# Performance work log

Measured on AMD Instinct MI355X. Metric: run time of the kernel, lower is better.

The kernel has to match this reference:

```python
import jax, jax.numpy as jnp
import numpy as np


def setup_inputs() -> dict:
    key = jax.random.key(0)
    k1, k2, k3 = jax.random.split(key, 3)
    B, C, H, W = 16, 512, 64, 64
    K = 32
    std = 1.0 / (K * C) ** 0.5
    x = jax.random.normal(k1, (B, C, H, W), dtype=jnp.float32)
    codewords = jax.random.uniform(k2, (K, C), dtype=jnp.float32, minval=-std, maxval=std)
    scale = jax.random.uniform(k3, (K,), dtype=jnp.float32, minval=-1.0, maxval=0.0)
    return {"x": x, "codewords": codewords, "scale": scale}


def reference(x, codewords, scale):
    # x: [B, C, H, W] -> tokens [B, N, C] with N = H*W
    B, C, H, W = x.shape
    xf = x.reshape(B, C, H * W).transpose(0, 2, 1)  # [B, N, C]

    # (avoids materializing the [B, N, K, C] tensor the torch code builds)
    x_sq = jnp.sum(xf * xf, axis=-1)                 # [B, N]
    c_sq = jnp.sum(codewords * codewords, axis=-1)   # [K]
    xc = jnp.einsum('bnc,kc->bnk', xf, codewords)    # [B, N, K]
    scaled_l2 = scale * (x_sq[..., None] - 2.0 * xc + c_sq)  # [B, N, K]

    w = jax.nn.softmax(scaled_l2, axis=2)            # [B, N, K]

    # aggregate: sum_n w[b,n,k] * (x[b,n,:] - c[k,:])
    #          = einsum(w, x) - (sum_n w) * c
    enc = jnp.einsum('bnk,bnc->bkc', w, xf) - jnp.sum(w, axis=1)[..., None] * codewords
    return enc  # [B, K, C]
```

## Files before the change

### kernel.cpp

```cpp
#include <hip/hip_runtime.h>


#define B_ 16
#define C_ 512
#define N_ 4096
#define K_ 32
#define CWS 520
#define WLS 40
#define XCP 132

typedef __attribute__((ext_vector_type(8))) short short8;
typedef __attribute__((ext_vector_type(16))) float floatx16;

__device__ inline unsigned short f2bf(float f) {
    union { float f; unsigned u; } v; v.f = f;
    unsigned r = v.u + 0x7FFFu + ((v.u >> 16) & 1u);
    return (unsigned short)(r >> 16);
}
__device__ inline float bf2f(unsigned short s) {
    union { unsigned u; float f; } v; v.u = ((unsigned)s) << 16;
    return v.f;
}

template <int USE_WS>
__global__ __launch_bounds__(256, 2)
void enc_kernel(const float* __restrict__ x, const float* __restrict__ cw,
                const float* __restrict__ scale, float* __restrict__ outp)
{
    __shared__ unsigned short cwT[K_ * CWS];
    __shared__ unsigned short XC[2][64 * XCP];
    __shared__ unsigned short Wl[4][K_ * WLS];
    __shared__ float xsqp[4][128];
    __shared__ float csq[K_];
    __shared__ float scl[K_];

    const int tid  = threadIdx.x;
    const int wave = tid >> 6;
    const int lane = tid & 63;
    const int l31  = lane & 31;
    const int lh   = lane >> 5;

    const int b     = blockIdx.x >> 5;
    const int chunk = blockIdx.x & 31;
    const float* xb = x + (long)b * C_ * N_;

    const int r = tid >> 5;
    const int p = tid & 31;
    const float* xrow = xb + chunk * 128 + p * 4;

    float4 sA[8], sB[8];
#define XISSUE(buf_, g_)                                                       \
    { _Pragma("unroll")                                                        \
      for (int i = 0; i < 8; ++i)                                              \
          buf_[i] = *(const float4*)(xrow + (long)((g_) * 64 + i * 8 + r) * N_); }

    float xs0 = 0.f, xs1 = 0.f, xs2 = 0.f, xs3 = 0.f;
#define XWRITE(buf_, dst_)                                                     \
    { _Pragma("unroll")                                                        \
      for (int i = 0; i < 8; ++i) {                                            \
          const float4 v = buf_[i];                                            \
          xs0 += v.x * v.x; xs1 += v.y * v.y;                                  \
          xs2 += v.z * v.z; xs3 += v.w * v.w;                                  \
          const unsigned lo = (unsigned)f2bf(v.x) | ((unsigned)f2bf(v.y) << 16);\
          const unsigned hi = (unsigned)f2bf(v.z) | ((unsigned)f2bf(v.w) << 16);\
          *(uint2*)&XC[dst_][(i * 8 + r) * XCP + p * 4] = make_uint2(lo, hi);  \
      } }

    XISSUE(sA, 0)
    XISSUE(sB, 1)

    if (tid < K_) scl[tid] = scale[tid];
    {
        const int k = tid >> 3, q = tid & 7;
        const float4* src = (const float4*)(cw + k * C_ + q * 64);
        float s = 0.f;
        #pragma unroll
        for (int i = 0; i < 16; ++i) {
            const float4 v = src[i];
            s += v.x*v.x + v.y*v.y + v.z*v.z + v.w*v.w;
            const unsigned lo = (unsigned)f2bf(v.x) | ((unsigned)f2bf(v.y) << 16);
            const unsigned hi = (unsigned)f2bf(v.z) | ((unsigned)f2bf(v.w) << 16);
            *(uint2*)&cwT[k * CWS + q * 64 + i * 4] = make_uint2(lo, hi);
        }
        s += __shfl_xor(s, 1); s += __shfl_xor(s, 2); s += __shfl_xor(s, 4);
        if (q == 0) csq[k] = s;
    }

    XWRITE(sA, 0)
    __syncthreads();

    floatx16 S;
    #pragma unroll
    for (int i = 0; i < 16; ++i) S[i] = 0.f;

    #pragma unroll
    for (int g = 0; g < 8; ++g) {
        if (g + 2 < 8) {
            if ((g & 1) == 0) { XISSUE(sA, g + 2) } else { XISSUE(sB, g + 2) }
        }
        #pragma unroll
        for (int s = 0; s < 4; ++s) {
            const short8 af = *(const short8*)&cwT[l31 * CWS + (g * 4 + s) * 16 + lh * 8];
            short8 bx;
            #pragma unroll
            for (int j = 0; j < 8; ++j)
                bx[j] = (short)XC[g & 1][(s * 16 + lh * 8 + j) * XCP + wave * 32 + l31];
            S = __builtin_amdgcn_mfma_f32_32x32x16_bf16(af, bx, S, 0, 0, 0);
        }
        if (g + 1 < 8) {
            if ((g & 1) == 0) { XWRITE(sB, (g + 1) & 1) } else { XWRITE(sA, (g + 1) & 1) }
        }
        if (g < 7) __syncthreads();
    }

    xs0 += __shfl_xor(xs0, 32); xs1 += __shfl_xor(xs1, 32);
    xs2 += __shfl_xor(xs2, 32); xs3 += __shfl_xor(xs3, 32);
    if (lane < 32) {
        xsqp[wave][l31 * 4 + 0] = xs0; xsqp[wave][l31 * 4 + 1] = xs1;
        xsqp[wave][l31 * 4 + 2] = xs2; xsqp[wave][l31 * 4 + 3] = xs3;
    }

    float4 bv[6][2];
#define G2LOAD(bi_, i_)                                                        \
    { const int t_ = (i_) >> 3, st_ = (i_) & 7;                                \
      const int c_ = wave * 128 + t_ * 32 + l31;                               \
      const int no_ = (st_ >> 1) * 32 + (st_ & 1) * 16 + lh * 8;               \
      const float* p_ = xb + (long)c_ * N_ + chunk * 128 + no_;                \
      bv[bi_][0] = *(const float4*)p_;                                         \
      bv[bi_][1] = *(const float4*)(p_ + 4); }
    G2LOAD(0, 0)
    G2LOAD(1, 1)
    G2LOAD(2, 2)
    G2LOAD(3, 3)
    G2LOAD(4, 4)
    G2LOAD(5, 5)

    __syncthreads();

    {
        const int n = wave * 32 + l31;
        const float xq = xsqp[0][n] + xsqp[1][n] + xsqp[2][n] + xsqp[3][n];
        float L[16], mx = -3.4e38f;
        #pragma unroll
        for (int rr = 0; rr < 16; ++rr) {
            const int k = (rr & 3) + 8 * (rr >> 2) + 4 * lh;
            L[rr] = scl[k] * (xq - 2.f * S[rr] + csq[k]);
            mx = fmaxf(mx, L[rr]);
        }
        mx = fmaxf(mx, __shfl_xor(mx, 32));
        float sum = 0.f;
        #pragma unroll
        for (int rr = 0; rr < 16; ++rr) { L[rr] = __expf(L[rr] - mx); sum += L[rr]; }
        sum += __shfl_xor(sum, 32);
        const float inv = 1.f / sum;
        #pragma unroll
        for (int rr = 0; rr < 16; ++rr) {
            const int k = (rr & 3) + 8 * (rr >> 2) + 4 * lh;
            Wl[wave][k * WLS + l31] = f2bf(L[rr] * inv);
        }
    }
    __syncthreads();

    short8 aw[8];
    #pragma unroll
    for (int st = 0; st < 8; ++st)
        aw[st] = *(const short8*)&Wl[st >> 1][l31 * WLS + (st & 1) * 16 + lh * 8];

    floatx16 wacc;
    #pragma unroll
    for (int i = 0; i < 16; ++i) wacc[i] = 0.f;
    {
        short8 ones;
        #pragma unroll
        for (int j = 0; j < 8; ++j) ones[j] = (short)0x3F80;
        #pragma unroll
        for (int st = 0; st < 8; ++st)
            wacc = __builtin_amdgcn_mfma_f32_32x32x16_bf16(aw[st], ones, wacc, 0, 0, 0);
    }

    floatx16 acc[4];
    #pragma unroll
    for (int t = 0; t < 4; ++t)
        #pragma unroll
        for (int i = 0; i < 16; ++i) acc[t][i] = 0.f;

    #pragma unroll
    for (int i = 0; i < 32; ++i) {
        const int bi = i % 6;
        const int t  = i >> 3, st = i & 7;
        const float4 v0 = bv[bi][0];
        const float4 v1 = bv[bi][1];
        short8 bx;
        bx[0] = (short)f2bf(v0.x); bx[1] = (short)f2bf(v0.y);
        bx[2] = (short)f2bf(v0.z); bx[3] = (short)f2bf(v0.w);
        bx[4] = (short)f2bf(v1.x); bx[5] = (short)f2bf(v1.y);
        bx[6] = (short)f2bf(v1.z); bx[7] = (short)f2bf(v1.w);
        acc[t] = __builtin_amdgcn_mfma_f32_32x32x16_bf16(aw[st], bx, acc[t], 0, 0, 0);
        if (i + 6 < 32) G2LOAD(bi, i + 6)
    }

    float* dst = USE_WS ? (outp + (size_t)blockIdx.x * K_ * C_)
                        : (outp + (size_t)b * K_ * C_);
    #pragma unroll
    for (int t = 0; t < 4; ++t) {
        const int c = wave * 128 + t * 32 + l31;
        #pragma unroll
        for (int rr = 0; rr < 16; ++rr) {
            const int k = (rr & 3) + 8 * (rr >> 2) + 4 * lh;
            const float cwv = bf2f(cwT[k * CWS + c]);
            const float val = acc[t][rr] - wacc[rr] * cwv;
            if (USE_WS) dst[k * C_ + c] = val;
            else        atomicAdd(dst + k * C_ + c, val);
        }
    }
}

__global__ __launch_bounds__(256)
void reduce_kernel(const float4* __restrict__ part, float4* __restrict__ out)
{
    const int gid = blockIdx.x * 256 + threadIdx.x;
    const int bb  = gid >> 12;
    const int i4  = gid & 4095;
    const float4* p = part + ((size_t)bb * 32) * 4096 + i4;
    float4 s = make_float4(0.f, 0.f, 0.f, 0.f);
    #pragma unroll
    for (int ch = 0; ch < 32; ++ch) {
        const float4 v = p[(size_t)ch * 4096];
        s.x += v.x; s.y += v.y; s.z += v.z; s.w += v.w;
    }
    out[gid] = s;
}

extern "C" void kernel_launch(void* const* d_in, const int* in_sizes, int n_in,
                              void* d_out, int out_size, void* d_ws, size_t ws_size,
                              hipStream_t stream) {
    const float* x     = (const float*)d_in[0];
    const float* cw    = (const float*)d_in[1];
    const float* scale = (const float*)d_in[2];
    float* out = (float*)d_out;

    const size_t ws_need = (size_t)512 * K_ * C_ * sizeof(float);
    if (ws_size >= ws_need) {
        float* part = (float*)d_ws;
        hipLaunchKernelGGL(enc_kernel<1>, dim3(B_ * 32), dim3(256), 0, stream,
                           x, cw, scale, part);
        hipLaunchKernelGGL(reduce_kernel, dim3(256), dim3(256), 0, stream,
                           (const float4*)part, (float4*)out);
    } else {
        hipMemsetAsync(out, 0, (size_t)out_size * sizeof(float), stream);
        hipLaunchKernelGGL(enc_kernel<0>, dim3(B_ * 32), dim3(256), 0, stream,
                           x, cw, scale, out);
    }
}
```

Baseline: 216.7 us.

## Halve token chunk, keep whole x tile in LDS, precompute bf16 codewords

Token chunk per block drops from 128 to 64, doubling the block count to 1024. The full 512x64 bf16 x tile now stays resident in LDS, so the aggregation GEMM reads it from LDS instead of re-reading x from global memory a second time. Codeword bf16 conversion and norms move to a tiny separate kernel, and the distance MFMAs run on two waves that load A fragments from global. The trade-offs are an extra launch, a partial-sum workspace twice as large for the reduce kernel, and idle waves during the first GEMM.

```diff
diff --git a/kernel.cpp b/kernel.cpp
--- a/kernel.cpp
+++ b/kernel.cpp
@@ -5,9 +5,11 @@
 #define C_ 512
 #define N_ 4096
 #define K_ 32
-#define CWS 520
+#define CHUNK 64
+#define NCH (N_ / CHUNK)
+#define NBLK (B_ * NCH)
+#define XCP 72
 #define WLS 40
-#define XCP 132
 
 typedef __attribute__((ext_vector_type(8))) short short8;
 typedef __attribute__((ext_vector_type(16))) float floatx16;
@@ -17,20 +19,39 @@
     unsigned r = v.u + 0x7FFFu + ((v.u >> 16) & 1u);
     return (unsigned short)(r >> 16);
 }
-__device__ inline float bf2f(unsigned short s) {
-    union { unsigned u; float f; } v; v.u = ((unsigned)s) << 16;
-    return v.f;
+
+__global__ __launch_bounds__(256)
+void cw_convert(const float* __restrict__ cw, unsigned short* __restrict__ cwb,
+                float* __restrict__ csq)
+{
+    const int tid = threadIdx.x;
+    const int k = tid >> 3, q = tid & 7;
+    const float4* src = (const float4*)(cw + k * C_ + q * 64);
+    float s = 0.f;
+    #pragma unroll
+    for (int i = 0; i < 16; ++i) {
+        const float4 v = src[i];
+        s += v.x*v.x + v.y*v.y + v.z*v.z + v.w*v.w;
+        const unsigned lo = (unsigned)f2bf(v.x) | ((unsigned)f2bf(v.y) << 16);
+        const unsigned hi = (unsigned)f2bf(v.z) | ((unsigned)f2bf(v.w) << 16);
+        *(uint2*)&cwb[k * C_ + q * 64 + i * 4] = make_uint2(lo, hi);
+    }
+    s += __shfl_xor(s, 1); s += __shfl_xor(s, 2); s += __shfl_xor(s, 4);
+    if (q == 0) csq[k] = s;
 }
 
 template <int USE_WS>
 __global__ __launch_bounds__(256, 2)
-void enc_kernel(const float* __restrict__ x, const float* __restrict__ cw,
-                const float* __restrict__ scale, float* __restrict__ outp)
+void enc_kernel(const float* __restrict__ x,
+                const unsigned short* __restrict__ cwb,
+                const float* __restrict__ csqg,
+                const float* __restrict__ cw,
+                const float* __restrict__ scale,
+                float* __restrict__ outp)
 {
-    __shared__ unsigned short cwT[K_ * CWS];
-    __shared__ unsigned short XC[2][64 * XCP];
-    __shared__ unsigned short Wl[4][K_ * WLS];
-    __shared__ float xsqp[4][128];
+    __shared__ unsigned short XC[C_ * XCP];
+    __shared__ unsigned short Wl[2][K_ * WLS];
+    __shared__ float xsqp[4][CHUNK];
     __shared__ float csq[K_];
     __shared__ float scl[K_];
 
@@ -40,53 +61,46 @@
     const int l31  = lane & 31;
     const int lh   = lane >> 5;
 
-    const int b     = blockIdx.x >> 5;
-    const int chunk = blockIdx.x & 31;
+    const int b     = blockIdx.x >> 6;
+    const int chunk = blockIdx.x & (NCH - 1);
     const float* xb = x + (long)b * C_ * N_;
 
-    const int r = tid >> 5;
-    const int p = tid & 31;
-    const float* xrow = xb + chunk * 128 + p * 4;
-
-    float4 sA[8], sB[8];
+    const int r = tid >> 4;
+    const int p = tid & 15;
+    const float* xrow = xb + chunk * CHUNK + p * 4;
+
+    if (tid < K_) { scl[tid] = scale[tid]; csq[tid] = csqg[tid]; }
+
+    float4 s0[4], s1[4], s2[4];
 #define XISSUE(buf_, g_)                                                       \
     { _Pragma("unroll")                                                        \
-      for (int i = 0; i < 8; ++i)                                              \
-          buf_[i] = *(const float4*)(xrow + (long)((g_) * 64 + i * 8 + r) * N_); }
+      for (int i = 0; i < 4; ++i)                                              \
+          buf_[i] = *(const float4*)(xrow + (long)((g_) * 64 + i * 16 + r) * N_); }
 
     float xs0 = 0.f, xs1 = 0.f, xs2 = 0.f, xs3 = 0.f;
-#define XWRITE(buf_, dst_)                                                     \
+#define XWRITE(buf_, g_)                                                       \
     { _Pragma("unroll")                                                        \
-      for (int i = 0; i < 8; ++i) {                                            \
+      for (int i = 0; i < 4; ++i) {                                            \
           const float4 v = buf_[i];                                            \
           xs0 += v.x * v.x; xs1 += v.y * v.y;                                  \
           xs2 += v.z * v.z; xs3 += v.w * v.w;                                  \
           const unsigned lo = (unsigned)f2bf(v.x) | ((unsigned)f2bf(v.y) << 16);\
           const unsigned hi = (unsigned)f2bf(v.z) | ((unsigned)f2bf(v.w) << 16);\
-          *(uint2*)&XC[dst_][(i * 8 + r) * XCP + p * 4] = make_uint2(lo, hi);  \
+          *(uint2*)&XC[((g_) * 64 + i * 16 + r) * XCP + p * 4] = make_uint2(lo, hi);\
       } }
 
-    XISSUE(sA, 0)
-    XISSUE(sB, 1)
-
-    if (tid < K_) scl[tid] = scale[tid];
-    {
-        const int k = tid >> 3, q = tid & 7;
-        const float4* src = (const float4*)(cw + k * C_ + q * 64);
-        float s = 0.f;
-        #pragma unroll
-        for (int i = 0; i < 16; ++i) {
-            const float4 v = src[i];
-            s += v.x*v.x + v.y*v.y + v.z*v.z + v.w*v.w;
-            const unsigned lo = (unsigned)f2bf(v.x) | ((unsigned)f2bf(v.y) << 16);
-            const unsigned hi = (unsigned)f2bf(v.z) | ((unsigned)f2bf(v.w) << 16);
-            *(uint2*)&cwT[k * CWS + q * 64 + i * 4] = make_uint2(lo, hi);
-        }
-        s += __shfl_xor(s, 1); s += __shfl_xor(s, 2); s += __shfl_xor(s, 4);
-        if (q == 0) csq[k] = s;
-    }
-
-    XWRITE(sA, 0)
+    const unsigned short* cwr = cwb + l31 * C_ + lh * 8;
+    short8 afA[4], afB[4];
+#define AFLOAD(buf_, g_)                                                       \
+    { _Pragma("unroll")                                                        \
+      for (int s = 0; s < 4; ++s)                                              \
+          buf_[s] = *(const short8*)(cwr + (g_) * 64 + s * 16); }
+
+    XISSUE(s0, 0)
+    XISSUE(s1, 1)
+    if (wave < 2) AFLOAD(afA, 0)
+    XWRITE(s0, 0)
+    XISSUE(s2, 2)
     __syncthreads();
 
     floatx16 S;
@@ -95,49 +109,44 @@
 
     #pragma unroll
     for (int g = 0; g < 8; ++g) {
-        if (g + 2 < 8) {
-            if ((g & 1) == 0) { XISSUE(sA, g + 2) } else { XISSUE(sB, g + 2) }
-        }
-        #pragma unroll
-        for (int s = 0; s < 4; ++s) {
-            const short8 af = *(const short8*)&cwT[l31 * CWS + (g * 4 + s) * 16 + lh * 8];
-            short8 bx;
+        if (g + 3 < 8) {
+            if      ((g % 3) == 0) XISSUE(s0, g + 3)
+            else if ((g % 3) == 1) XISSUE(s1, g + 3)
+            else                   XISSUE(s2, g + 3)
+        }
+        if (wave < 2) {
+            if (g + 1 < 8) {
+                if (g & 1) AFLOAD(afA, g + 1) else AFLOAD(afB, g + 1)
+            }
             #pragma unroll
-            for (int j = 0; j < 8; ++j)
-                bx[j] = (short)XC[g & 1][(s * 16 + lh * 8 + j) * XCP + wave * 32 + l31];
-            S = __builtin_amdgcn_mfma_f32_32x32x16_bf16(af, bx, S, 0, 0, 0);
+            for (int s = 0; s < 4; ++s) {
+                short8 bx;
+                #pragma unroll
+                for (int j = 0; j < 8; ++j)
+                    bx[j] = (short)XC[(g * 64 + s * 16 + lh * 8 + j) * XCP + wave * 32 + l31];
+                S = __builtin_amdgcn_mfma_f32_32x32x16_bf16((g & 1) ? afB[s] : afA[s],
+                                                            bx, S, 0, 0, 0);
+            }
         }
         if (g + 1 < 8) {
-            if ((g & 1) == 0) { XWRITE(sB, (g + 1) & 1) } else { XWRITE(sA, (g + 1) & 1) }
+            if      (((g + 1) % 3) == 0) XWRITE(s0, g + 1)
+            else if (((g + 1) % 3) == 1) XWRITE(s1, g + 1)
+            else                         XWRITE(s2, g + 1)
         }
         if (g < 7) __syncthreads();
     }
 
+    xs0 += __shfl_xor(xs0, 16); xs1 += __shfl_xor(xs1, 16);
+    xs2 += __shfl_xor(xs2, 16); xs3 += __shfl_xor(xs3, 16);
     xs0 += __shfl_xor(xs0, 32); xs1 += __shfl_xor(xs1, 32);
     xs2 += __shfl_xor(xs2, 32); xs3 += __shfl_xor(xs3, 32);
-    if (lane < 32) {
-        xsqp[wave][l31 * 4 + 0] = xs0; xsqp[wave][l31 * 4 + 1] = xs1;
-        xsqp[wave][l31 * 4 + 2] = xs2; xsqp[wave][l31 * 4 + 3] = xs3;
-    }
-
-    float4 bv[6][2];
-#define G2LOAD(bi_, i_)                                                        \
-    { const int t_ = (i_) >> 3, st_ = (i_) & 7;                                \
-      const int c_ = wave * 128 + t_ * 32 + l31;                               \
-      const int no_ = (st_ >> 1) * 32 + (st_ & 1) * 16 + lh * 8;               \
-      const float* p_ = xb + (long)c_ * N_ + chunk * 128 + no_;                \
-      bv[bi_][0] = *(const float4*)p_;                                         \
-      bv[bi_][1] = *(const float4*)(p_ + 4); }
-    G2LOAD(0, 0)
-    G2LOAD(1, 1)
-    G2LOAD(2, 2)
-    G2LOAD(3, 3)
-    G2LOAD(4, 4)
-    G2LOAD(5, 5)
-
+    if (lane < 16) {
+        xsqp[wave][lane * 4 + 0] = xs0; xsqp[wave][lane * 4 + 1] = xs1;
+        xsqp[wave][lane * 4 + 2] = xs2; xsqp[wave][lane * 4 + 3] = xs3;
+    }
     __syncthreads();
 
-    {
+    if (wave < 2) {
         const int n = wave * 32 + l31;
         const float xq = xsqp[0][n] + xsqp[1][n] + xsqp[2][n] + xsqp[3][n];
         float L[16], mx = -3.4e38f;
@@ -161,10 +170,10 @@
     }
     __syncthreads();
 
-    short8 aw[8];
-    #pragma unroll
-    for (int st = 0; st < 8; ++st)
-        aw[st] = *(const short8*)&Wl[st >> 1][l31 * WLS + (st & 1) * 16 + lh * 8];
+    short8 aw[4];
+    #pragma unroll
+    for (int s = 0; s < 4; ++s)
+        aw[s] = *(const short8*)&Wl[s >> 1][l31 * WLS + (s & 1) * 16 + lh * 8];
 
     floatx16 wacc;
     #pragma unroll
@@ -174,8 +183,8 @@
         #pragma unroll
         for (int j = 0; j < 8; ++j) ones[j] = (short)0x3F80;
         #pragma unroll
-        for (int st = 0; st < 8; ++st)
-            wacc = __builtin_amdgcn_mfma_f32_32x32x16_bf16(aw[st], ones, wacc, 0, 0, 0);
+        for (int s = 0; s < 4; ++s)
+            wacc = __builtin_amdgcn_mfma_f32_32x32x16_bf16(aw[s], ones, wacc, 0, 0, 0);
     }
 
     floatx16 acc[4];
@@ -185,18 +194,13 @@
         for (int i = 0; i < 16; ++i) acc[t][i] = 0.f;
 
     #pragma unroll
-    for (int i = 0; i < 32; ++i) {
-        const int bi = i % 6;
-        const int t  = i >> 3, st = i & 7;
-        const float4 v0 = bv[bi][0];
-        const float4 v1 = bv[bi][1];
-        short8 bx;
-        bx[0] = (short)f2bf(v0.x); bx[1] = (short)f2bf(v0.y);
-        bx[2] = (short)f2bf(v0.z); bx[3] = (short)f2bf(v0.w);
-        bx[4] = (short)f2bf(v1.x); bx[5] = (short)f2bf(v1.y);
-        bx[6] = (short)f2bf(v1.z); bx[7] = (short)f2bf(v1.w);
-        acc[t] = __builtin_amdgcn_mfma_f32_32x32x16_bf16(aw[st], bx, acc[t], 0, 0, 0);
-        if (i + 6 < 32) G2LOAD(bi, i + 6)
+    for (int t = 0; t < 4; ++t) {
+        const int c = wave * 128 + t * 32 + l31;
+        #pragma unroll
+        for (int s = 0; s < 4; ++s) {
+            const short8 bx = *(const short8*)&XC[c * XCP + s * 16 + lh * 8];
+            acc[t] = __builtin_amdgcn_mfma_f32_32x32x16_bf16(aw[s], bx, acc[t], 0, 0, 0);
+        }
     }
 
     float* dst = USE_WS ? (outp + (size_t)blockIdx.x * K_ * C_)
@@ -207,8 +211,7 @@
         #pragma unroll
         for (int rr = 0; rr < 16; ++rr) {
             const int k = (rr & 3) + 8 * (rr >> 2) + 4 * lh;
-            const float cwv = bf2f(cwT[k * CWS + c]);
-            const float val = acc[t][rr] - wacc[rr] * cwv;
+            const float val = acc[t][rr] - wacc[rr] * cw[k * C_ + c];
             if (USE_WS) dst[k * C_ + c] = val;
             else        atomicAdd(dst + k * C_ + c, val);
         }
@@ -221,10 +224,10 @@
     const int gid = blockIdx.x * 256 + threadIdx.x;
     const int bb  = gid >> 12;
     const int i4  = gid & 4095;
-    const float4* p = part + ((size_t)bb * 32) * 4096 + i4;
+    const float4* p = part + ((size_t)bb * NCH) * 4096 + i4;
     float4 s = make_float4(0.f, 0.f, 0.f, 0.f);
-    #pragma unroll
-    for (int ch = 0; ch < 32; ++ch) {
+    #pragma unroll 8
+    for (int ch = 0; ch < NCH; ++ch) {
         const float4 v = p[(size_t)ch * 4096];
         s.x += v.x; s.y += v.y; s.z += v.z; s.w += v.w;
     }
@@ -239,16 +242,22 @@
     const float* scale = (const float*)d_in[2];
     float* out = (float*)d_out;
 
-    const size_t ws_need = (size_t)512 * K_ * C_ * sizeof(float);
+    unsigned short* cwb = (unsigned short*)d_ws;
+    float* csq = (float*)((char*)d_ws + (size_t)K_ * C_ * sizeof(unsigned short));
+    const size_t part_off = 65536;
+    const size_t ws_need = part_off + (size_t)NBLK * K_ * C_ * sizeof(float);
+
     if (ws_size >= ws_need) {
-        float* part = (float*)d_ws;
-        hipLaunchKernelGGL(enc_kernel<1>, dim3(B_ * 32), dim3(256), 0, stream,
-                           x, cw, scale, part);
+        float* part = (float*)((char*)d_ws + part_off);
+        hipLaunchKernelGGL(cw_convert, dim3(1), dim3(256), 0, stream, cw, cwb, csq);
+        hipLaunchKernelGGL(enc_kernel<1>, dim3(NBLK), dim3(256), 0, stream,
+                           x, cwb, csq, cw, scale, part);
         hipLaunchKernelGGL(reduce_kernel, dim3(256), dim3(256), 0, stream,
                            (const float4*)part, (float4*)out);
     } else {
         hipMemsetAsync(out, 0, (size_t)out_size * sizeof(float), stream);
-        hipLaunchKernelGGL(enc_kernel<0>, dim3(B_ * 32), dim3(256), 0, stream,
-                           x, cw, scale, out);
-    }
-}
+        hipLaunchKernelGGL(cw_convert, dim3(1), dim3(256), 0, stream, cw, cwb, csq);
+        hipLaunchKernelGGL(enc_kernel<0>, dim3(NBLK), dim3(256), 0, stream,
+                           x, cwb, csq, cw, scale, out);
+    }
+}
```

Result: slower. 222.9 us (+2.9%).

## Drop LDS staging; load x and codewords directly from global into MFMA operands

Applied to the files above, without the earlier changes.

Removes the shared-memory staging of bf16 x tiles and the transposed codeword table. Each lane now loads its x column elements and codeword fragments straight from global memory, converting to bf16 in registers, and computes the x-squared norm per lane, which eliminates the cross-wave xsqp reduction. This frees LDS so occupancy can rise to 3 blocks per CU, and replaces __syncthreads with lighter custom barriers. The cost is strided scalar global loads for x (one float per row, 8 rows per MFMA) with no software prefetch, and redundant codeword reads across waves, which may expose memory latency.

```diff
diff --git a/kernel.cpp b/kernel.cpp
--- a/kernel.cpp
+++ b/kernel.cpp
@@ -5,9 +5,10 @@
 #define C_ 512
 #define N_ 4096
 #define K_ 32
-#define CWS 520
+#define CHUNK 128
+#define NCH (N_ / CHUNK)
+#define NBLK (B_ * NCH)
 #define WLS 40
-#define XCP 132
 
 typedef __attribute__((ext_vector_type(8))) short short8;
 typedef __attribute__((ext_vector_type(16))) float floatx16;
@@ -17,20 +18,22 @@
     unsigned r = v.u + 0x7FFFu + ((v.u >> 16) & 1u);
     return (unsigned short)(r >> 16);
 }
-__device__ inline float bf2f(unsigned short s) {
-    union { unsigned u; float f; } v; v.u = ((unsigned)s) << 16;
-    return v.f;
+
+__device__ inline void cbar() {
+    __builtin_amdgcn_sched_barrier(0);
+    asm volatile("s_waitcnt lgkmcnt(0)" ::: "memory");
+    __builtin_amdgcn_s_barrier();
+    __builtin_amdgcn_sched_barrier(0);
 }
 
 template <int USE_WS>
-__global__ __launch_bounds__(256, 2)
-void enc_kernel(const float* __restrict__ x, const float* __restrict__ cw,
-                const float* __restrict__ scale, float* __restrict__ outp)
+__global__ __launch_bounds__(256, 3)
+void enc_kernel(const float* __restrict__ x,
+                const float* __restrict__ cw,
+                const float* __restrict__ scale,
+                float* __restrict__ outp)
 {
-    __shared__ unsigned short cwT[K_ * CWS];
-    __shared__ unsigned short XC[2][64 * XCP];
     __shared__ unsigned short Wl[4][K_ * WLS];
-    __shared__ float xsqp[4][128];
     __shared__ float csq[K_];
     __shared__ float scl[K_];
 
@@ -41,91 +44,79 @@
     const int lh   = lane >> 5;
 
     const int b     = blockIdx.x >> 5;
-    const int chunk = blockIdx.x & 31;
+    const int chunk = blockIdx.x & (NCH - 1);
     const float* xb = x + (long)b * C_ * N_;
-
-    const int r = tid >> 5;
-    const int p = tid & 31;
-    const float* xrow = xb + chunk * 128 + p * 4;
-
-    float4 sA[8], sB[8];
-#define XISSUE(buf_, g_)                                                       \
-    { _Pragma("unroll")                                                        \
-      for (int i = 0; i < 8; ++i)                                              \
-          buf_[i] = *(const float4*)(xrow + (long)((g_) * 64 + i * 8 + r) * N_); }
-
-    float xs0 = 0.f, xs1 = 0.f, xs2 = 0.f, xs3 = 0.f;
-#define XWRITE(buf_, dst_)                                                     \
-    { _Pragma("unroll")                                                        \
-      for (int i = 0; i < 8; ++i) {                                            \
-          const float4 v = buf_[i];                                            \
-          xs0 += v.x * v.x; xs1 += v.y * v.y;                                  \
-          xs2 += v.z * v.z; xs3 += v.w * v.w;                                  \
-          const unsigned lo = (unsigned)f2bf(v.x) | ((unsigned)f2bf(v.y) << 16);\
-          const unsigned hi = (unsigned)f2bf(v.z) | ((unsigned)f2bf(v.w) << 16);\
-          *(uint2*)&XC[dst_][(i * 8 + r) * XCP + p * 4] = make_uint2(lo, hi);  \
-      } }
-
-    XISSUE(sA, 0)
-    XISSUE(sB, 1)
 
     if (tid < K_) scl[tid] = scale[tid];
     {
         const int k = tid >> 3, q = tid & 7;
         const float4* src = (const float4*)(cw + k * C_ + q * 64);
-        float s = 0.f;
+        float ssum = 0.f;
         #pragma unroll
         for (int i = 0; i < 16; ++i) {
             const float4 v = src[i];
-            s += v.x*v.x + v.y*v.y + v.z*v.z + v.w*v.w;
-            const unsigned lo = (unsigned)f2bf(v.x) | ((unsigned)f2bf(v.y) << 16);
-            const unsigned hi = (unsigned)f2bf(v.z) | ((unsigned)f2bf(v.w) << 16);
-            *(uint2*)&cwT[k * CWS + q * 64 + i * 4] = make_uint2(lo, hi);
-        }
-        s += __shfl_xor(s, 1); s += __shfl_xor(s, 2); s += __shfl_xor(s, 4);
-        if (q == 0) csq[k] = s;
-    }
-
-    XWRITE(sA, 0)
-    __syncthreads();
+            ssum += v.x*v.x + v.y*v.y + v.z*v.z + v.w*v.w;
+        }
+        ssum += __shfl_xor(ssum, 1);
+        ssum += __shfl_xor(ssum, 2);
+        ssum += __shfl_xor(ssum, 4);
+        if (q == 0) csq[k] = ssum;
+    }
+
+    const float* xcol = xb + chunk * CHUNK + wave * 32 + l31;
+    const float* cwr  = cw + l31 * C_ + lh * 8;
+
+    short8 afA[4], afB[4];
+#define AFLOADG(buf_, ptr_)                                                    \
+    { _Pragma("unroll")                                                        \
+      for (int s = 0; s < 4; ++s) {                                            \
+          const float4 u0 = *(const float4*)((ptr_) + s * 16);                 \
+          const float4 u1 = *(const float4*)((ptr_) + s * 16 + 4);             \
+          short8 t_;                                                           \
+          t_[0] = (short)f2bf(u0.x); t_[1] = (short)f2bf(u0.y);                \
+          t_[2] = (short)f2bf(u0.z); t_[3] = (short)f2bf(u0.w);                \
+          t_[4] = (short)f2bf(u1.x); t_[5] = (short)f2bf(u1.y);                \
+          t_[6] = (short)f2bf(u1.z); t_[7] = (short)f2bf(u1.w);                \
+          buf_[s] = t_; } }
 
     floatx16 S;
     #pragma unroll
     for (int i = 0; i < 16; ++i) S[i] = 0.f;
-
-    #pragma unroll
+    float xs = 0.f;
+
+    AFLOADG(afA, cwr)
+    #pragma unroll 2
     for (int g = 0; g < 8; ++g) {
-        if (g + 2 < 8) {
-            if ((g & 1) == 0) { XISSUE(sA, g + 2) } else { XISSUE(sB, g + 2) }
+        const float* xg = xcol + (long)g * 64 * N_;
+        if (g + 1 < 8) {
+            if (g & 1) AFLOADG(afA, cwr + (g + 1) * 64)
+            else       AFLOADG(afB, cwr + (g + 1) * 64)
         }
         #pragma unroll
         for (int s = 0; s < 4; ++s) {
-            const short8 af = *(const short8*)&cwT[l31 * CWS + (g * 4 + s) * 16 + lh * 8];
+            float xv[8];
+            #pragma unroll
+            for (int j = 0; j < 8; ++j)
+                xv[j] = xg[(long)(s * 16 + lh * 8 + j) * N_];
             short8 bx;
             #pragma unroll
-            for (int j = 0; j < 8; ++j)
-                bx[j] = (short)XC[g & 1][(s * 16 + lh * 8 + j) * XCP + wave * 32 + l31];
-            S = __builtin_amdgcn_mfma_f32_32x32x16_bf16(af, bx, S, 0, 0, 0);
-        }
-        if (g + 1 < 8) {
-            if ((g & 1) == 0) { XWRITE(sB, (g + 1) & 1) } else { XWRITE(sA, (g + 1) & 1) }
-        }
-        if (g < 7) __syncthreads();
-    }
-
-    xs0 += __shfl_xor(xs0, 32); xs1 += __shfl_xor(xs1, 32);
-    xs2 += __shfl_xor(xs2, 32); xs3 += __shfl_xor(xs3, 32);
-    if (lane < 32) {
-        xsqp[wave][l31 * 4 + 0] = xs0; xsqp[wave][l31 * 4 + 1] = xs1;
-        xsqp[wave][l31 * 4 + 2] = xs2; xsqp[wave][l31 * 4 + 3] = xs3;
-    }
+            for (int j = 0; j < 8; ++j) {
+                xs += xv[j] * xv[j];
+                bx[j] = (short)f2bf(xv[j]);
+            }
+            S = __builtin_amdgcn_mfma_f32_32x32x16_bf16(
+                    (g & 1) ? afB[s] : afA[s], bx, S, 0, 0, 0);
+        }
+    }
+
+    xs += __shfl_xor(xs, 32);
 
     float4 bv[6][2];
 #define G2LOAD(bi_, i_)                                                        \
     { const int t_ = (i_) >> 3, st_ = (i_) & 7;                                \
       const int c_ = wave * 128 + t_ * 32 + l31;                               \
       const int no_ = (st_ >> 1) * 32 + (st_ & 1) * 16 + lh * 8;               \
-      const float* p_ = xb + (long)c_ * N_ + chunk * 128 + no_;                \
+      const float* p_ = xb + (long)c_ * N_ + chunk * CHUNK + no_;              \
       bv[bi_][0] = *(const float4*)p_;                                         \
       bv[bi_][1] = *(const float4*)(p_ + 4); }
     G2LOAD(0, 0)
@@ -135,11 +126,10 @@
     G2LOAD(4, 4)
     G2LOAD(5, 5)
 
-    __syncthreads();
+    cbar();
 
     {
-        const int n = wave * 32 + l31;
-        const float xq = xsqp[0][n] + xsqp[1][n] + xsqp[2][n] + xsqp[3][n];
+        const float xq = xs;
         float L[16], mx = -3.4e38f;
         #pragma unroll
         for (int rr = 0; rr < 16; ++rr) {
@@ -159,7 +149,7 @@
             Wl[wave][k * WLS + l31] = f2bf(L[rr] * inv);
         }
     }
-    __syncthreads();
+    cbar();
 
     short8 aw[8];
     #pragma unroll
@@ -207,8 +197,7 @@
         #pragma unroll
         for (int rr = 0; rr < 16; ++rr) {
             const int k = (rr & 3) + 8 * (rr >> 2) + 4 * lh;
-            const float cwv = bf2f(cwT[k * CWS + c]);
-            const float val = acc[t][rr] - wacc[rr] * cwv;
+            const float val = acc[t][rr] - wacc[rr] * cw[k * C_ + c];
             if (USE_WS) dst[k * C_ + c] = val;
             else        atomicAdd(dst + k * C_ + c, val);
         }
@@ -221,11 +210,11 @@
     const int gid = blockIdx.x * 256 + threadIdx.x;
     const int bb  = gid >> 12;
     const int i4  = gid & 4095;
-    const float4* p = part + ((size_t)bb * 32) * 4096 + i4;
+    const float4* pp = part + ((size_t)bb * NCH) * 4096 + i4;
     float4 s = make_float4(0.f, 0.f, 0.f, 0.f);
     #pragma unroll
-    for (int ch = 0; ch < 32; ++ch) {
-        const float4 v = p[(size_t)ch * 4096];
+    for (int j = 0; j < NCH; ++j) {
+        const float4 v = pp[(size_t)j * 4096];
         s.x += v.x; s.y += v.y; s.z += v.z; s.w += v.w;
     }
     out[gid] = s;
@@ -239,16 +228,16 @@
     const float* scale = (const float*)d_in[2];
     float* out = (float*)d_out;
 
-    const size_t ws_need = (size_t)512 * K_ * C_ * sizeof(float);
+    const size_t ws_need = (size_t)NBLK * K_ * C_ * sizeof(float);
     if (ws_size >= ws_need) {
         float* part = (float*)d_ws;
-        hipLaunchKernelGGL(enc_kernel<1>, dim3(B_ * 32), dim3(256), 0, stream,
+        hipLaunchKernelGGL(enc_kernel<1>, dim3(NBLK), dim3(256), 0, stream,
                            x, cw, scale, part);
         hipLaunchKernelGGL(reduce_kernel, dim3(256), dim3(256), 0, stream,
                            (const float4*)part, (float4*)out);
     } else {
         hipMemsetAsync(out, 0, (size_t)out_size * sizeof(float), stream);
-        hipLaunchKernelGGL(enc_kernel<0>, dim3(B_ * 32), dim3(256), 0, stream,
+        hipLaunchKernelGGL(enc_kernel<0>, dim3(NBLK), dim3(256), 0, stream,
                            x, cw, scale, out);
     }
 }
```

Measured after the change: 223.3 us. +3.0%, slower.
